# Kernel optimization log

Hardware: AMD Instinct MI355X
Metric: run time of the kernel (lower is better)

The kernel has to match this reference:

```python
import jax, jax.numpy as jnp
import numpy as np

N_NODES = 50000

def gcn_conv(x, W, b, src, dst, n):
    # PyG GCNConv: h = x @ W; add self-loops; sym-normalized mean aggregation; + bias
    h = x @ W  # [N, out]
    deg = jax.ops.segment_sum(jnp.ones(src.shape[0], x.dtype), dst, num_segments=n) + 1.0  # +1 self-loop
    dinv = jax.lax.rsqrt(deg)  # deg^{-1/2}
    norm = dinv[src] * dinv[dst]  # [E]
    msg = h[src] * norm[:, None]  # [E, out]
    agg = jax.ops.segment_sum(msg, dst, num_segments=n)
    agg = agg + h * (dinv * dinv)[:, None]  # self-loop contribution, norm = 1/deg
    return agg + b


def setup_inputs() -> dict:
    key = jax.random.key(0)
    ks = jax.random.split(key, 12)
    f1, h1, h2, a = 128, 128, 64, N_NODES
    def glorot(k, shape):
        lim = float(np.sqrt(6.0 / (shape[0] + shape[1])))
        return jax.random.uniform(k, shape, jnp.float32, -lim, lim)
    x = jax.random.normal(ks[0], (N_NODES, f1), jnp.float32)
    edge_index = jax.random.randint(ks[1], (2, 800000), 0, N_NODES, dtype=jnp.int64)
    W1 = glorot(ks[2], (f1, h1)); b1 = jnp.zeros((h1,), jnp.float32)
    W2 = glorot(ks[3], (h1, h2)); b2 = jnp.zeros((h2,), jnp.float32)
    W3 = glorot(ks[4], (h2, 1));  b3 = jnp.zeros((1,), jnp.float32)
    lim4 = float(1.0 / np.sqrt(a))
    W4 = jax.random.uniform(ks[5], (a,), jnp.float32, -lim4, lim4)
    b4 = jax.random.uniform(ks[6], (1,), jnp.float32, -lim4, lim4)
    return {"x": x, "edge_index": edge_index, "W1": W1, "b1": b1,
            "W2": W2, "b2": b2, "W3": W3, "b3": b3, "W4": W4, "b4": b4}


def reference(x, edge_index, W1, b1, W2, b2, W3, b3, W4, b4):
    src, dst = edge_index[0], edge_index[1]
    n = x.shape[0]
    h = jnp.tanh(gcn_conv(x, W1, b1, src, dst, n))
    h = jnp.tanh(gcn_conv(h, W2, b2, src, dst, n))
    h = jnp.tanh(gcn_conv(h, W3, b3, src, dst, n))
    h = h.reshape(-1)  # [N] == action_dim
    out = jnp.dot(W4, h) + b4  # Linear(action_dim, 1) -> [1]
    return out
```

## Files before the change

### kernel.cpp

```cpp
#include <hip/hip_runtime.h>
#include <math.h>


constexpr int BLOCK = 256;
constexpr int SLOTS = 64;

__global__ void slot_fill(const int* __restrict__ src, const int* __restrict__ dst,
                          int* __restrict__ deg, unsigned short* __restrict__ slots, int E) {
    int base = (blockIdx.x * blockDim.x + threadIdx.x) * 4;
    if (base + 4 <= E) {
        int4 d4 = *reinterpret_cast<const int4*>(dst + base);
        int4 s4 = *reinterpret_cast<const int4*>(src + base);
        int p0 = atomicAdd(&deg[d4.x], 1);
        int p1 = atomicAdd(&deg[d4.y], 1);
        int p2 = atomicAdd(&deg[d4.z], 1);
        int p3 = atomicAdd(&deg[d4.w], 1);
        if (p0 < SLOTS) slots[(size_t)d4.x * SLOTS + p0] = (unsigned short)s4.x;
        if (p1 < SLOTS) slots[(size_t)d4.y * SLOTS + p1] = (unsigned short)s4.y;
        if (p2 < SLOTS) slots[(size_t)d4.z * SLOTS + p2] = (unsigned short)s4.z;
        if (p3 < SLOTS) slots[(size_t)d4.w * SLOTS + p3] = (unsigned short)s4.w;
    } else {
        for (int e = base; e < E; ++e) {
            int d = dst[e];
            int p = atomicAdd(&deg[d], 1);
            if (p < SLOTS) slots[(size_t)d * SLOTS + p] = (unsigned short)src[e];
        }
    }
}

template<int K, int M>
__global__ void __launch_bounds__(256) gemm_tiled(const float* __restrict__ X,
                                                  const float* __restrict__ W,
                                                  const int* __restrict__ deg,
                                                  float* __restrict__ H, int N) {
    constexpr int BM = 64;
    constexpr int TN = 4;
    constexpr int TX = M / TN;
    constexpr int TY = 256 / TX;
    constexpr int TM = BM / TY;
    constexpr int K4 = K / 4;

    __shared__ float xs[BM][K];

    const int tid = threadIdx.x;
    const int n0 = blockIdx.x * BM;

    {
        const float4* X4 = reinterpret_cast<const float4*>(X);
        constexpr int F4_PER_ROW = K / 4;
        constexpr int TOT = BM * F4_PER_ROW;
#pragma unroll
        for (int i = 0; i < TOT / 256; ++i) {
            int idx = tid + i * 256;
            int row = idx / F4_PER_ROW;
            int k4 = idx % F4_PER_ROW;
            float4 v = make_float4(0.f, 0.f, 0.f, 0.f);
            if (n0 + row < N) v = X4[(size_t)(n0 + row) * F4_PER_ROW + k4];
            *reinterpret_cast<float4*>(&xs[row][k4 * 4]) = v;
        }
    }
    __syncthreads();

    const int tx = tid % TX;
    const int ty = tid / TX;
    const int col0 = tx * TN;
    const int row0 = ty * TM;

    float acc[TM][TN];
#pragma unroll
    for (int r = 0; r < TM; ++r)
#pragma unroll
        for (int c = 0; c < TN; ++c) acc[r][c] = 0.0f;

    const float4* W4 = reinterpret_cast<const float4*>(W);
    constexpr int W4_PER_ROW = M / 4;

#pragma unroll 4
    for (int k4 = 0; k4 < K4; ++k4) {
        float4 wv[4];
#pragma unroll
        for (int i = 0; i < 4; ++i)
            wv[i] = W4[(size_t)(k4 * 4 + i) * W4_PER_ROW + tx];
        float4 xv[TM];
#pragma unroll
        for (int r = 0; r < TM; ++r)
            xv[r] = *reinterpret_cast<const float4*>(&xs[row0 + r][k4 * 4]);
#pragma unroll
        for (int r = 0; r < TM; ++r) {
#pragma unroll
            for (int c = 0; c < TN; ++c) {
                acc[r][c] = fmaf(xv[r].x, ((float*)&wv[0])[c], acc[r][c]);
                acc[r][c] = fmaf(xv[r].y, ((float*)&wv[1])[c], acc[r][c]);
                acc[r][c] = fmaf(xv[r].z, ((float*)&wv[2])[c], acc[r][c]);
                acc[r][c] = fmaf(xv[r].w, ((float*)&wv[3])[c], acc[r][c]);
            }
        }
    }

#pragma unroll
    for (int r = 0; r < TM; ++r) {
        int row = n0 + row0 + r;
        if (row < N) {
            float di = 1.0f / sqrtf((float)deg[row] + 1.0f);
            float4 o;
            o.x = acc[r][0] * di; o.y = acc[r][1] * di;
            o.z = acc[r][2] * di; o.w = acc[r][3] * di;
            *reinterpret_cast<float4*>(&H[(size_t)row * M + col0]) = o;
        }
    }
}

__global__ void __launch_bounds__(256) agg128(const int* __restrict__ deg,
                                              const unsigned short* __restrict__ slots,
                                              const float* __restrict__ Hs,
                                              const float* __restrict__ bias,
                                              float* __restrict__ A, int N) {
    int wid = threadIdx.x >> 6;
    int lane = threadIdx.x & 63;
    int n = blockIdx.x * 4 + wid;
    if (n >= N) return;
    int half = lane >> 5, sub = lane & 31;
    const float4* H4 = reinterpret_cast<const float4*>(Hs);
    float4 acc = make_float4(0.f, 0.f, 0.f, 0.f);
    if (half == 0) acc = H4[(size_t)n * 32 + sub];
    int dg = deg[n];
    int cnt = min(dg, SLOTS);
    int idxv = (lane < cnt) ? (int)slots[(size_t)n * SLOTS + lane] : N;
    int cnt16 = (cnt + 15) & ~15;
    for (int j = 0; j < cnt16; j += 16) {
        int s0 = __shfl(idxv, j + half);
        int s1 = __shfl(idxv, j + 2 + half);
        int s2 = __shfl(idxv, j + 4 + half);
        int s3 = __shfl(idxv, j + 6 + half);
        int s4 = __shfl(idxv, j + 8 + half);
        int s5 = __shfl(idxv, j + 10 + half);
        int s6 = __shfl(idxv, j + 12 + half);
        int s7 = __shfl(idxv, j + 14 + half);
        float4 v0 = H4[(size_t)s0 * 32 + sub];
        float4 v1 = H4[(size_t)s1 * 32 + sub];
        float4 v2 = H4[(size_t)s2 * 32 + sub];
        float4 v3 = H4[(size_t)s3 * 32 + sub];
        float4 v4 = H4[(size_t)s4 * 32 + sub];
        float4 v5 = H4[(size_t)s5 * 32 + sub];
        float4 v6 = H4[(size_t)s6 * 32 + sub];
        float4 v7 = H4[(size_t)s7 * 32 + sub];
        acc.x += (v0.x + v1.x) + (v2.x + v3.x) + (v4.x + v5.x) + (v6.x + v7.x);
        acc.y += (v0.y + v1.y) + (v2.y + v3.y) + (v4.y + v5.y) + (v6.y + v7.y);
        acc.z += (v0.z + v1.z) + (v2.z + v3.z) + (v4.z + v5.z) + (v6.z + v7.z);
        acc.w += (v0.w + v1.w) + (v2.w + v3.w) + (v4.w + v5.w) + (v6.w + v7.w);
    }
    acc.x += __shfl_down(acc.x, 32);
    acc.y += __shfl_down(acc.y, 32);
    acc.z += __shfl_down(acc.z, 32);
    acc.w += __shfl_down(acc.w, 32);
    if (half == 0) {
        float di = 1.0f / sqrtf((float)dg + 1.0f);
        float4 b = reinterpret_cast<const float4*>(bias)[sub];
        float4 o;
        o.x = tanhf(acc.x * di + b.x);
        o.y = tanhf(acc.y * di + b.y);
        o.z = tanhf(acc.z * di + b.z);
        o.w = tanhf(acc.w * di + b.w);
        reinterpret_cast<float4*>(A)[(size_t)n * 32 + sub] = o;
    }
}

__global__ void __launch_bounds__(256) agg64_dot3(const int* __restrict__ deg,
                                                  const unsigned short* __restrict__ slots,
                                                  const float* __restrict__ Hs,
                                                  const float* __restrict__ b2,
                                                  const float* __restrict__ W3,
                                                  float* __restrict__ Hs3, int N) {
    int wid = threadIdx.x >> 6;
    int lane = threadIdx.x & 63;
    int n = blockIdx.x * 4 + wid;
    if (n >= N) return;
    int grp = lane >> 4, sub = lane & 15;
    const float4* H4 = reinterpret_cast<const float4*>(Hs);
    float4 acc = make_float4(0.f, 0.f, 0.f, 0.f);
    if (grp == 0) acc = H4[(size_t)n * 16 + sub];
    int dg = deg[n];
    int cnt = min(dg, SLOTS);
    int idxv = (lane < cnt) ? (int)slots[(size_t)n * SLOTS + lane] : N;
    int cnt16 = (cnt + 15) & ~15;
    int j = 0;
    for (; j + 32 <= cnt16; j += 32) {
        int s0 = __shfl(idxv, j + grp);
        int s1 = __shfl(idxv, j + 4 + grp);
        int s2 = __shfl(idxv, j + 8 + grp);
        int s3 = __shfl(idxv, j + 12 + grp);
        int s4 = __shfl(idxv, j + 16 + grp);
        int s5 = __shfl(idxv, j + 20 + grp);
        int s6 = __shfl(idxv, j + 24 + grp);
        int s7 = __shfl(idxv, j + 28 + grp);
        float4 v0 = H4[(size_t)s0 * 16 + sub];
        float4 v1 = H4[(size_t)s1 * 16 + sub];
        float4 v2 = H4[(size_t)s2 * 16 + sub];
        float4 v3 = H4[(size_t)s3 * 16 + sub];
        float4 v4 = H4[(size_t)s4 * 16 + sub];
        float4 v5 = H4[(size_t)s5 * 16 + sub];
        float4 v6 = H4[(size_t)s6 * 16 + sub];
        float4 v7 = H4[(size_t)s7 * 16 + sub];
        acc.x += (v0.x + v1.x) + (v2.x + v3.x) + (v4.x + v5.x) + (v6.x + v7.x);
        acc.y += (v0.y + v1.y) + (v2.y + v3.y) + (v4.y + v5.y) + (v6.y + v7.y);
        acc.z += (v0.z + v1.z) + (v2.z + v3.z) + (v4.z + v5.z) + (v6.z + v7.z);
        acc.w += (v0.w + v1.w) + (v2.w + v3.w) + (v4.w + v5.w) + (v6.w + v7.w);
    }
    for (; j < cnt16; j += 16) {
        int s0 = __shfl(idxv, j + grp);
        int s1 = __shfl(idxv, j + 4 + grp);
        int s2 = __shfl(idxv, j + 8 + grp);
        int s3 = __shfl(idxv, j + 12 + grp);
        float4 v0 = H4[(size_t)s0 * 16 + sub];
        float4 v1 = H4[(size_t)s1 * 16 + sub];
        float4 v2 = H4[(size_t)s2 * 16 + sub];
        float4 v3 = H4[(size_t)s3 * 16 + sub];
        acc.x += (v0.x + v1.x) + (v2.x + v3.x);
        acc.y += (v0.y + v1.y) + (v2.y + v3.y);
        acc.z += (v0.z + v1.z) + (v2.z + v3.z);
        acc.w += (v0.w + v1.w) + (v2.w + v3.w);
    }
    acc.x += __shfl_xor(acc.x, 16);
    acc.y += __shfl_xor(acc.y, 16);
    acc.z += __shfl_xor(acc.z, 16);
    acc.w += __shfl_xor(acc.w, 16);
    acc.x += __shfl_xor(acc.x, 32);
    acc.y += __shfl_xor(acc.y, 32);
    acc.z += __shfl_xor(acc.z, 32);
    acc.w += __shfl_xor(acc.w, 32);
    float di = 1.0f / sqrtf((float)dg + 1.0f);
    float4 b = reinterpret_cast<const float4*>(b2)[sub];
    float4 w = reinterpret_cast<const float4*>(W3)[sub];
    float t = tanhf(acc.x * di + b.x) * w.x
            + tanhf(acc.y * di + b.y) * w.y
            + tanhf(acc.z * di + b.z) * w.z
            + tanhf(acc.w * di + b.w) * w.w;
#pragma unroll
    for (int off = 1; off < 16; off <<= 1) t += __shfl_xor(t, off);
    if (lane == 0) Hs3[n] = t * di;
}

__global__ void __launch_bounds__(256) agg_dot(const int* __restrict__ deg,
                                               const unsigned short* __restrict__ slots,
                                               const float* __restrict__ Hs,
                                               const float* __restrict__ b3,
                                               const float* __restrict__ W4,
                                               float* __restrict__ partials, int N) {
    __shared__ float sm[4];
    int wid = threadIdx.x >> 6;
    int lane = threadIdx.x & 63;
    int n = blockIdx.x * 4 + wid;
    float p = 0.0f;
    if (n < N) {
        int dg = deg[n];
        int cnt = min(dg, SLOTS);
        float acc = (lane < cnt) ? Hs[(int)slots[(size_t)n * SLOTS + lane]] : 0.0f;
#pragma unroll
        for (int off = 32; off > 0; off >>= 1) acc += __shfl_down(acc, off);
        if (lane == 0) {
            float di = 1.0f / sqrtf((float)dg + 1.0f);
            float h = tanhf((acc + Hs[n]) * di + b3[0]);
            p = W4[n] * h;
        }
    }
    if (lane == 0) sm[wid] = p;
    __syncthreads();
    if (threadIdx.x == 0) partials[blockIdx.x] = sm[0] + sm[1] + sm[2] + sm[3];
}

__global__ void final_sum(const float* __restrict__ partials, int B,
                          const float* __restrict__ b4, float* __restrict__ out) {
    float acc = 0.0f;
    for (int i = threadIdx.x; i < B; i += blockDim.x) acc += partials[i];
#pragma unroll
    for (int off = 32; off > 0; off >>= 1) acc += __shfl_down(acc, off);
    __shared__ float sm[4];
    int lane = threadIdx.x & 63, wid = threadIdx.x >> 6;
    if (lane == 0) sm[wid] = acc;
    __syncthreads();
    if (threadIdx.x == 0) out[0] = sm[0] + sm[1] + sm[2] + sm[3] + b4[0];
}

extern "C" void kernel_launch(void* const* d_in, const int* in_sizes, int n_in,
                              void* d_out, int out_size, void* d_ws, size_t ws_size,
                              hipStream_t stream) {
    const float* x  = (const float*)d_in[0];
    const int*   ei = (const int*)d_in[1];
    const float* W1 = (const float*)d_in[2];
    const float* b1 = (const float*)d_in[3];
    const float* W2 = (const float*)d_in[4];
    const float* b2 = (const float*)d_in[5];
    const float* W3 = (const float*)d_in[6];
    const float* b3 = (const float*)d_in[7];
    const float* W4 = (const float*)d_in[8];
    const float* b4 = (const float*)d_in[9];

    const int N = in_sizes[0] / 128;
    const int E = in_sizes[1] / 2;
    const int* src = ei;
    const int* dst = ei + E;

    const int nblkW = (N + 3) / 4;

    float* base = (float*)d_ws;
    size_t off = 0;
    auto alloc = [&](size_t cnt, size_t align_f) -> float* {
        off = (off + align_f - 1) / align_f * align_f;
        float* p = base + off;
        off += cnt;
        return p;
    };
    int* deg     = (int*)alloc(N, 1);
    unsigned short* slots = (unsigned short*)alloc((size_t)N * SLOTS / 2, 64);
    float* bufA  = alloc((size_t)(N + 1) * 128, 64);
    float* bufB  = alloc((size_t)N * 128, 64);
    float* partials = alloc(nblkW, 64);

    float* hs2 = bufA;

    const int nblkE4 = (E / 4 + BLOCK - 1) / BLOCK + 1;
    const int ngemm = (N + 63) / 64;

    hipMemsetAsync(deg, 0, (size_t)N * sizeof(int), stream);
    hipMemsetAsync(bufA + (size_t)N * 128, 0, 128 * sizeof(float), stream);
    slot_fill<<<nblkE4, BLOCK, 0, stream>>>(src, dst, deg, slots, E);

    gemm_tiled<128, 128><<<ngemm, 256, 0, stream>>>(x, W1, deg, bufA, N);
    agg128<<<nblkW, 256, 0, stream>>>(deg, slots, bufA, b1, bufB, N);

    gemm_tiled<128, 64><<<ngemm, 256, 0, stream>>>(bufB, W2, deg, hs2, N);
    hipMemsetAsync(hs2 + (size_t)N * 64, 0, 64 * sizeof(float), stream);
    agg64_dot3<<<nblkW, 256, 0, stream>>>(deg, slots, hs2, b2, W3, bufB, N);

    agg_dot<<<nblkW, 256, 0, stream>>>(deg, slots, bufB, b3, W4, partials, N);
    final_sum<<<1, BLOCK, 0, stream>>>(partials, nblkW, b4, (float*)d_out);
}
```

Baseline: 303.0 us.

## Fuse slot fill with first GEMM and move source normalization into aggregation

The edge slot-fill (degree counting) is merged into the first GEMM launch by interleaving blocks: odd blocks do the atomic slot fill and even blocks compute x@W1 without normalization. Because the GEMM no longer depends on degrees, source-side deg^-1/2 scaling moves into agg128 as a per-neighbor gather of a precomputed dinv array. A small kernel precomputes dinv for all later stages. This removes one serialization point and lets the fill overlap the GEMM, at the cost of an extra dinv gather per neighbor in the first aggregation and one extra launch.

```diff
diff --git a/kernel.cpp b/kernel.cpp
--- a/kernel.cpp
+++ b/kernel.cpp
@@ -5,33 +5,123 @@
 constexpr int BLOCK = 256;
 constexpr int SLOTS = 64;
 
-__global__ void slot_fill(const int* __restrict__ src, const int* __restrict__ dst,
-                          int* __restrict__ deg, unsigned short* __restrict__ slots, int E) {
-    int base = (blockIdx.x * blockDim.x + threadIdx.x) * 4;
-    if (base + 4 <= E) {
-        int4 d4 = *reinterpret_cast<const int4*>(dst + base);
-        int4 s4 = *reinterpret_cast<const int4*>(src + base);
-        int p0 = atomicAdd(&deg[d4.x], 1);
-        int p1 = atomicAdd(&deg[d4.y], 1);
-        int p2 = atomicAdd(&deg[d4.z], 1);
-        int p3 = atomicAdd(&deg[d4.w], 1);
-        if (p0 < SLOTS) slots[(size_t)d4.x * SLOTS + p0] = (unsigned short)s4.x;
-        if (p1 < SLOTS) slots[(size_t)d4.y * SLOTS + p1] = (unsigned short)s4.y;
-        if (p2 < SLOTS) slots[(size_t)d4.z * SLOTS + p2] = (unsigned short)s4.z;
-        if (p3 < SLOTS) slots[(size_t)d4.w * SLOTS + p3] = (unsigned short)s4.w;
-    } else {
-        for (int e = base; e < E; ++e) {
-            int d = dst[e];
-            int p = atomicAdd(&deg[d], 1);
-            if (p < SLOTS) slots[(size_t)d * SLOTS + p] = (unsigned short)src[e];
-        }
-    }
+template<int K, int M>
+__global__ void __launch_bounds__(256) gemm1_fill(const float* __restrict__ X,
+                                                  const float* __restrict__ W,
+                                                  float* __restrict__ H, int N,
+                                                  const int* __restrict__ src,
+                                                  const int* __restrict__ dst,
+                                                  int* __restrict__ deg,
+                                                  unsigned short* __restrict__ slots,
+                                                  int E) {
+    __shared__ float xs[64][K];
+    if (blockIdx.x & 1) {
+        int blk = blockIdx.x >> 1;
+        int base = (blk * blockDim.x + threadIdx.x) * 4;
+        if (base + 4 <= E) {
+            int4 d4 = *reinterpret_cast<const int4*>(dst + base);
+            int4 s4 = *reinterpret_cast<const int4*>(src + base);
+            int p0 = atomicAdd(&deg[d4.x], 1);
+            int p1 = atomicAdd(&deg[d4.y], 1);
+            int p2 = atomicAdd(&deg[d4.z], 1);
+            int p3 = atomicAdd(&deg[d4.w], 1);
+            if (p0 < SLOTS) slots[(size_t)d4.x * SLOTS + p0] = (unsigned short)s4.x;
+            if (p1 < SLOTS) slots[(size_t)d4.y * SLOTS + p1] = (unsigned short)s4.y;
+            if (p2 < SLOTS) slots[(size_t)d4.z * SLOTS + p2] = (unsigned short)s4.z;
+            if (p3 < SLOTS) slots[(size_t)d4.w * SLOTS + p3] = (unsigned short)s4.w;
+        } else {
+            for (int e = base; e < E; ++e) {
+                int d = dst[e];
+                int p = atomicAdd(&deg[d], 1);
+                if (p < SLOTS) slots[(size_t)d * SLOTS + p] = (unsigned short)src[e];
+            }
+        }
+        return;
+    }
+    constexpr int BM = 64;
+    constexpr int TN = 4;
+    constexpr int TX = M / TN;
+    constexpr int TY = 256 / TX;
+    constexpr int TM = BM / TY;
+    constexpr int K4 = K / 4;
+
+    const int tid = threadIdx.x;
+    const int n0 = (blockIdx.x >> 1) * BM;
+
+    {
+        const float4* X4 = reinterpret_cast<const float4*>(X);
+        constexpr int F4_PER_ROW = K / 4;
+        constexpr int TOT = BM * F4_PER_ROW;
+#pragma unroll
+        for (int i = 0; i < TOT / 256; ++i) {
+            int idx = tid + i * 256;
+            int row = idx / F4_PER_ROW;
+            int k4 = idx % F4_PER_ROW;
+            float4 v = make_float4(0.f, 0.f, 0.f, 0.f);
+            if (n0 + row < N) v = X4[(size_t)(n0 + row) * F4_PER_ROW + k4];
+            *reinterpret_cast<float4*>(&xs[row][k4 * 4]) = v;
+        }
+    }
+    __syncthreads();
+
+    const int tx = tid % TX;
+    const int ty = tid / TX;
+    const int col0 = tx * TN;
+    const int row0 = ty * TM;
+
+    float acc[TM][TN];
+#pragma unroll
+    for (int r = 0; r < TM; ++r)
+#pragma unroll
+        for (int c = 0; c < TN; ++c) acc[r][c] = 0.0f;
+
+    const float4* W4 = reinterpret_cast<const float4*>(W);
+    constexpr int W4_PER_ROW = M / 4;
+
+#pragma unroll 4
+    for (int k4 = 0; k4 < K4; ++k4) {
+        float4 wv[4];
+#pragma unroll
+        for (int i = 0; i < 4; ++i)
+            wv[i] = W4[(size_t)(k4 * 4 + i) * W4_PER_ROW + tx];
+        float4 xv[TM];
+#pragma unroll
+        for (int r = 0; r < TM; ++r)
+            xv[r] = *reinterpret_cast<const float4*>(&xs[row0 + r][k4 * 4]);
+#pragma unroll
+        for (int r = 0; r < TM; ++r) {
+#pragma unroll
+            for (int c = 0; c < TN; ++c) {
+                acc[r][c] = fmaf(xv[r].x, ((float*)&wv[0])[c], acc[r][c]);
+                acc[r][c] = fmaf(xv[r].y, ((float*)&wv[1])[c], acc[r][c]);
+                acc[r][c] = fmaf(xv[r].z, ((float*)&wv[2])[c], acc[r][c]);
+                acc[r][c] = fmaf(xv[r].w, ((float*)&wv[3])[c], acc[r][c]);
+            }
+        }
+    }
+
+#pragma unroll
+    for (int r = 0; r < TM; ++r) {
+        int row = n0 + row0 + r;
+        if (row < N) {
+            float4 o;
+            o.x = acc[r][0]; o.y = acc[r][1];
+            o.z = acc[r][2]; o.w = acc[r][3];
+            *reinterpret_cast<float4*>(&H[(size_t)row * M + col0]) = o;
+        }
+    }
+}
+
+__global__ void dinv_kernel(const int* __restrict__ deg, float* __restrict__ dinv, int N) {
+    int i = blockIdx.x * blockDim.x + threadIdx.x;
+    if (i < N) dinv[i] = 1.0f / sqrtf((float)deg[i] + 1.0f);
+    else if (i == N) dinv[N] = 0.0f;
 }
 
 template<int K, int M>
 __global__ void __launch_bounds__(256) gemm_tiled(const float* __restrict__ X,
                                                   const float* __restrict__ W,
-                                                  const int* __restrict__ deg,
+                                                  const float* __restrict__ dinv,
                                                   float* __restrict__ H, int N) {
     constexpr int BM = 64;
     constexpr int TN = 4;
@@ -101,7 +191,7 @@
     for (int r = 0; r < TM; ++r) {
         int row = n0 + row0 + r;
         if (row < N) {
-            float di = 1.0f / sqrtf((float)deg[row] + 1.0f);
+            float di = dinv[row];
             float4 o;
             o.x = acc[r][0] * di; o.y = acc[r][1] * di;
             o.z = acc[r][2] * di; o.w = acc[r][3] * di;
@@ -112,6 +202,7 @@
 
 __global__ void __launch_bounds__(256) agg128(const int* __restrict__ deg,
                                               const unsigned short* __restrict__ slots,
+                                              const float* __restrict__ dinv,
                                               const float* __restrict__ Hs,
                                               const float* __restrict__ bias,
                                               float* __restrict__ A, int N) {
@@ -121,10 +212,13 @@
     if (n >= N) return;
     int half = lane >> 5, sub = lane & 31;
     const float4* H4 = reinterpret_cast<const float4*>(Hs);
+    float din = dinv[n];
     float4 acc = make_float4(0.f, 0.f, 0.f, 0.f);
-    if (half == 0) acc = H4[(size_t)n * 32 + sub];
-    int dg = deg[n];
-    int cnt = min(dg, SLOTS);
+    if (half == 0) {
+        float4 v = H4[(size_t)n * 32 + sub];
+        acc.x = din * v.x; acc.y = din * v.y; acc.z = din * v.z; acc.w = din * v.w;
+    }
+    int cnt = min(deg[n], SLOTS);
     int idxv = (lane < cnt) ? (int)slots[(size_t)n * SLOTS + lane] : N;
     int cnt16 = (cnt + 15) & ~15;
     for (int j = 0; j < cnt16; j += 16) {
@@ -136,6 +230,8 @@
         int s5 = __shfl(idxv, j + 10 + half);
         int s6 = __shfl(idxv, j + 12 + half);
         int s7 = __shfl(idxv, j + 14 + half);
+        float d0 = dinv[s0], d1 = dinv[s1], d2 = dinv[s2], d3 = dinv[s3];
+        float d4 = dinv[s4], d5 = dinv[s5], d6 = dinv[s6], d7 = dinv[s7];
         float4 v0 = H4[(size_t)s0 * 32 + sub];
         float4 v1 = H4[(size_t)s1 * 32 + sub];
         float4 v2 = H4[(size_t)s2 * 32 + sub];
@@ -144,29 +240,33 @@
         float4 v5 = H4[(size_t)s5 * 32 + sub];
         float4 v6 = H4[(size_t)s6 * 32 + sub];
         float4 v7 = H4[(size_t)s7 * 32 + sub];
-        acc.x += (v0.x + v1.x) + (v2.x + v3.x) + (v4.x + v5.x) + (v6.x + v7.x);
-        acc.y += (v0.y + v1.y) + (v2.y + v3.y) + (v4.y + v5.y) + (v6.y + v7.y);
-        acc.z += (v0.z + v1.z) + (v2.z + v3.z) + (v4.z + v5.z) + (v6.z + v7.z);
-        acc.w += (v0.w + v1.w) + (v2.w + v3.w) + (v4.w + v5.w) + (v6.w + v7.w);
+        acc.x += (fmaf(d0, v0.x, d1 * v1.x) + fmaf(d2, v2.x, d3 * v3.x))
+               + (fmaf(d4, v4.x, d5 * v5.x) + fmaf(d6, v6.x, d7 * v7.x));
+        acc.y += (fmaf(d0, v0.y, d1 * v1.y) + fmaf(d2, v2.y, d3 * v3.y))
+               + (fmaf(d4, v4.y, d5 * v5.y) + fmaf(d6, v6.y, d7 * v7.y));
+        acc.z += (fmaf(d0, v0.z, d1 * v1.z) + fmaf(d2, v2.z, d3 * v3.z))
+               + (fmaf(d4, v4.z, d5 * v5.z) + fmaf(d6, v6.z, d7 * v7.z));
+        acc.w += (fmaf(d0, v0.w, d1 * v1.w) + fmaf(d2, v2.w, d3 * v3.w))
+               + (fmaf(d4, v4.w, d5 * v5.w) + fmaf(d6, v6.w, d7 * v7.w));
     }
     acc.x += __shfl_down(acc.x, 32);
     acc.y += __shfl_down(acc.y, 32);
     acc.z += __shfl_down(acc.z, 32);
     acc.w += __shfl_down(acc.w, 32);
     if (half == 0) {
-        float di = 1.0f / sqrtf((float)dg + 1.0f);
         float4 b = reinterpret_cast<const float4*>(bias)[sub];
         float4 o;
-        o.x = tanhf(acc.x * di + b.x);
-        o.y = tanhf(acc.y * di + b.y);
-        o.z = tanhf(acc.z * di + b.z);
-        o.w = tanhf(acc.w * di + b.w);
+        o.x = tanhf(acc.x * din + b.x);
+        o.y = tanhf(acc.y * din + b.y);
+        o.z = tanhf(acc.z * din + b.z);
+        o.w = tanhf(acc.w * din + b.w);
         reinterpret_cast<float4*>(A)[(size_t)n * 32 + sub] = o;
     }
 }
 
 __global__ void __launch_bounds__(256) agg64_dot3(const int* __restrict__ deg,
                                                   const unsigned short* __restrict__ slots,
+                                                  const float* __restrict__ dinv,
                                                   const float* __restrict__ Hs,
                                                   const float* __restrict__ b2,
                                                   const float* __restrict__ W3,
@@ -179,8 +279,7 @@
     const float4* H4 = reinterpret_cast<const float4*>(Hs);
     float4 acc = make_float4(0.f, 0.f, 0.f, 0.f);
     if (grp == 0) acc = H4[(size_t)n * 16 + sub];
-    int dg = deg[n];
-    int cnt = min(dg, SLOTS);
+    int cnt = min(deg[n], SLOTS);
     int idxv = (lane < cnt) ? (int)slots[(size_t)n * SLOTS + lane] : N;
     int cnt16 = (cnt + 15) & ~15;
     int j = 0;
@@ -228,7 +327,7 @@
     acc.y += __shfl_xor(acc.y, 32);
     acc.z += __shfl_xor(acc.z, 32);
     acc.w += __shfl_xor(acc.w, 32);
-    float di = 1.0f / sqrtf((float)dg + 1.0f);
+    float di = dinv[n];
     float4 b = reinterpret_cast<const float4*>(b2)[sub];
     float4 w = reinterpret_cast<const float4*>(W3)[sub];
     float t = tanhf(acc.x * di + b.x) * w.x
@@ -242,6 +341,7 @@
 
 __global__ void __launch_bounds__(256) agg_dot(const int* __restrict__ deg,
                                                const unsigned short* __restrict__ slots,
+                                               const float* __restrict__ dinv,
                                                const float* __restrict__ Hs,
                                                const float* __restrict__ b3,
                                                const float* __restrict__ W4,
@@ -252,14 +352,12 @@
     int n = blockIdx.x * 4 + wid;
     float p = 0.0f;
     if (n < N) {
-        int dg = deg[n];
-        int cnt = min(dg, SLOTS);
+        int cnt = min(deg[n], SLOTS);
         float acc = (lane < cnt) ? Hs[(int)slots[(size_t)n * SLOTS + lane]] : 0.0f;
 #pragma unroll
         for (int off = 32; off > 0; off >>= 1) acc += __shfl_down(acc, off);
         if (lane == 0) {
-            float di = 1.0f / sqrtf((float)dg + 1.0f);
-            float h = tanhf((acc + Hs[n]) * di + b3[0]);
+            float h = tanhf((acc + Hs[n]) * dinv[n] + b3[0]);
             p = W4[n] * h;
         }
     }
@@ -311,6 +409,7 @@
         return p;
     };
     int* deg     = (int*)alloc(N, 1);
+    float* dinv  = alloc(N + 1, 1);
     unsigned short* slots = (unsigned short*)alloc((size_t)N * SLOTS / 2, 64);
     float* bufA  = alloc((size_t)(N + 1) * 128, 64);
     float* bufB  = alloc((size_t)N * 128, 64);
@@ -318,20 +417,23 @@
 
     float* hs2 = bufA;
 
-    const int nblkE4 = (E / 4 + BLOCK - 1) / BLOCK + 1;
     const int ngemm = (N + 63) / 64;
+    const int nfill = (E / 4 + BLOCK - 1) / BLOCK + 1;
+    const int nfused = 2 * ((ngemm > nfill) ? ngemm : nfill);
+    const int nblkN1 = (N + 1 + BLOCK - 1) / BLOCK;
 
     hipMemsetAsync(deg, 0, (size_t)N * sizeof(int), stream);
     hipMemsetAsync(bufA + (size_t)N * 128, 0, 128 * sizeof(float), stream);
-    slot_fill<<<nblkE4, BLOCK, 0, stream>>>(src, dst, deg, slots, E);
-
-    gemm_tiled<128, 128><<<ngemm, 256, 0, stream>>>(x, W1, deg, bufA, N);
-    agg128<<<nblkW, 256, 0, stream>>>(deg, slots, bufA, b1, bufB, N);
-
-    gemm_tiled<128, 64><<<ngemm, 256, 0, stream>>>(bufB, W2, deg, hs2, N);
+    gemm1_fill<128, 128><<<nfused, 256, 0, stream>>>(x, W1, bufA, N,
+                                                     src, dst, deg, slots, E);
+    dinv_kernel<<<nblkN1, BLOCK, 0, stream>>>(deg, dinv, N);
+
+    agg128<<<nblkW, 256, 0, stream>>>(deg, slots, dinv, bufA, b1, bufB, N);
+
+    gemm_tiled<128, 64><<<ngemm, 256, 0, stream>>>(bufB, W2, dinv, hs2, N);
     hipMemsetAsync(hs2 + (size_t)N * 64, 0, 64 * sizeof(float), stream);
-    agg64_dot3<<<nblkW, 256, 0, stream>>>(deg, slots, hs2, b2, W3, bufB, N);
-
-    agg_dot<<<nblkW, 256, 0, stream>>>(deg, slots, bufB, b3, W4, partials, N);
+    agg64_dot3<<<nblkW, 256, 0, stream>>>(deg, slots, dinv, hs2, b2, W3, bufB, N);
+
+    agg_dot<<<nblkW, 256, 0, stream>>>(deg, slots, dinv, bufB, b3, W4, partials, N);
     final_sum<<<1, BLOCK, 0, stream>>>(partials, nblkW, b4, (float*)d_out);
 }
```

Result: faster. 291.5 us (-3.8%).
